# Optimization experiments

Hardware: AMD Instinct MI355X
Metric: run time of the kernel (lower is better)

## Reference

```python
import jax, jax.numpy as jnp
import numpy as np

EMBED_DIM = 528
NUM_HEADS = 8
HEAD_DIM = EMBED_DIM // NUM_HEADS  # 66


def setup_inputs() -> dict:
    key = jax.random.key(0)
    k1, k2, k3, k4, k5 = jax.random.split(key, 5)
    B, D, H, W, C = 1, 16, 16, 16, EMBED_DIM
    s = 1.0 / np.sqrt(C)
    return {
        "x": jax.random.normal(k1, (B, D, H, W, C), dtype=jnp.float32),
        "w_qkv": jax.random.uniform(k2, (3 * C, C), dtype=jnp.float32, minval=-s, maxval=s),
        "b_qkv": jax.random.uniform(k3, (3 * C,), dtype=jnp.float32, minval=-s, maxval=s),
        "w_proj": jax.random.uniform(k4, (C, C), dtype=jnp.float32, minval=-s, maxval=s),
        "b_proj": jax.random.uniform(k5, (C,), dtype=jnp.float32, minval=-s, maxval=s),
    }


def reference(x, w_qkv, b_qkv, w_proj, b_proj):
    B, D, H, W, C = x.shape
    N = D * H * W
    h, hd = NUM_HEADS, HEAD_DIM
    scaling = hd ** (-0.5)

    xt = x.reshape(B, N, C)
    # qkv projection: [B, N, 3C] -> [3, B, h, N, hd]
    qkv = xt @ w_qkv.T + b_qkv
    qkv = qkv.reshape(B, N, 3, h, hd).transpose(2, 0, 3, 1, 4)
    q, k, v = qkv[0], qkv[1], qkv[2]

    # full attention over all D*H*W tokens
    attn = jnp.einsum('bhqd,bhkd->bhqk', q, k) * scaling
    attn = jax.nn.softmax(attn, axis=-1)
    out = jnp.einsum('bhqk,bhkd->bhqd', attn, v)  # [B, h, N, hd]

    out = out.transpose(0, 2, 1, 3).reshape(B, N, h * hd)
    out = out @ w_proj.T + b_proj
    return out.reshape(B, D, H, W, C)
```

## Files before the change

### kernel.cpp

```cpp
#include <hip/hip_runtime.h>

typedef __attribute__((ext_vector_type(8))) short bf16x8;
typedef __attribute__((ext_vector_type(4))) float f32x4;
typedef __attribute__((ext_vector_type(16))) float f32x16;

#define DEV __device__ __forceinline__

static constexpr int N_TOK = 4096;
static constexpr int C     = 528;
static constexpr int NH    = 8;
static constexpr int HD    = 66;
static constexpr int HDP   = 96;
static constexpr int VD96  = 96;
static constexpr int KP    = 544;
static constexpr int NQKV  = 1584;
static constexpr int NQKVP = 1632;

DEV unsigned short f2bf(float f) {
    unsigned int u = __float_as_uint(f);
    u = (u + 0x7fffu + ((u >> 16) & 1u)) >> 16;
    return (unsigned short)u;
}
DEV float bf2f(unsigned short h) { return __uint_as_float(((unsigned int)h) << 16); }
DEV unsigned cvtpk2(float a, float b) {
    unsigned r;
    asm("v_cvt_pk_bf16_f32 %0, %1, %2" : "=v"(r) : "v"(a), "v"(b));
    return r;
}
DEV void plswap(unsigned &a, unsigned &b) {
    asm volatile("v_permlane32_swap_b32 %0, %1" : "+v"(a), "+v"(b));
}

__global__ void k_prep_all(const float* __restrict__ x, const float* __restrict__ w_qkv,
                           const float* __restrict__ w_proj,
                           unsigned short* __restrict__ xb, unsigned short* __restrict__ wqkvb,
                           unsigned short* __restrict__ whi, unsigned short* __restrict__ wlo,
                           unsigned short* __restrict__ qb, unsigned short* __restrict__ kbuf) {
    const int T0 = N_TOK * KP;
    const int T1 = T0 + NQKVP * KP;
    const int T2 = T1 + KP * KP;
    const int T3 = T2 + NH * N_TOK * (HDP - HD);
    for (int idx = blockIdx.x * 256 + threadIdx.x; idx < T3; idx += gridDim.x * 256) {
        if (idx < T0) {
            int n = idx / KP, k = idx - n * KP;
            xb[idx] = (k < C) ? f2bf(x[n * C + k]) : (unsigned short)0;
        } else if (idx < T1) {
            int j = idx - T0;
            int n = j / KP, k = j - n * KP;
            wqkvb[j] = (n < NQKV && k < C) ? f2bf(w_qkv[n * C + k]) : (unsigned short)0;
        } else if (idx < T2) {
            int j = idx - T1;
            int n = j / KP, k = j - n * KP;
            unsigned short hi = 0, lo = 0;
            if (n < C && k < C) {
                float v = w_proj[n * C + k];
                hi = f2bf(v);
                lo = f2bf(v - bf2f(hi));
            }
            whi[j] = hi; wlo[j] = lo;
        } else {
            int j = idx - T2;
            int n = j / 30, p = j - 30 * n;
            size_t a = (size_t)n * HDP + HD + p;
            qb[a] = 0; kbuf[a] = 0;
        }
    }
}

__launch_bounds__(256)
__global__ void k_gemm_qkv(const unsigned short* __restrict__ A,
                           const unsigned short* __restrict__ B,
                           const float* __restrict__ bias,
                           unsigned short* __restrict__ qb, unsigned short* __restrict__ kbuf,
                           unsigned short* __restrict__ vtmp) {
    constexpr int LDA = 40;
    __shared__ unsigned short Al[2][128 * LDA];
    __shared__ unsigned short Bl[2][96 * LDA];
    int tid = threadIdx.x, lane = tid & 63, wid = tid >> 6;
    int m0 = blockIdx.x * 128, n0 = blockIdx.y * 96;
    int wm = (wid >> 1) * 64, wn = (wid & 1) * 48;
    int arow0 = tid >> 2, arow1 = (256 + tid) >> 2, akc = (tid & 3) * 8;
    bool bhave = tid < 128;
    int brow1 = (256 + tid) >> 2;
    f32x4 acc[4][3] = {};
    bf16x8 ra0, ra1, rb0, rb1;

    ra0 = *(const bf16x8*)&A[(size_t)(m0 + arow0) * KP + akc];
    ra1 = *(const bf16x8*)&A[(size_t)(m0 + arow1) * KP + akc];
    rb0 = *(const bf16x8*)&B[(size_t)(n0 + arow0) * KP + akc];
    if (bhave) rb1 = *(const bf16x8*)&B[(size_t)(n0 + brow1) * KP + akc];
    *(bf16x8*)&Al[0][arow0 * LDA + akc] = ra0;
    *(bf16x8*)&Al[0][arow1 * LDA + akc] = ra1;
    *(bf16x8*)&Bl[0][arow0 * LDA + akc] = rb0;
    if (bhave) *(bf16x8*)&Bl[0][brow1 * LDA + akc] = rb1;
    __syncthreads();

    int kk = (lane >> 4) * 8, cc = lane & 15;
    for (int kt = 0; kt < 17; kt++) {
        int cur = kt & 1;
        if (kt < 16) {
            int k0 = (kt + 1) * 32;
            ra0 = *(const bf16x8*)&A[(size_t)(m0 + arow0) * KP + k0 + akc];
            ra1 = *(const bf16x8*)&A[(size_t)(m0 + arow1) * KP + k0 + akc];
            rb0 = *(const bf16x8*)&B[(size_t)(n0 + arow0) * KP + k0 + akc];
            if (bhave) rb1 = *(const bf16x8*)&B[(size_t)(n0 + brow1) * KP + k0 + akc];
        }
        bf16x8 af[4], bfr[3];
#pragma unroll
        for (int mi = 0; mi < 4; mi++) af[mi] = *(const bf16x8*)&Al[cur][(wm + mi * 16 + cc) * LDA + kk];
#pragma unroll
        for (int ni = 0; ni < 3; ni++) bfr[ni] = *(const bf16x8*)&Bl[cur][(wn + ni * 16 + cc) * LDA + kk];
#pragma unroll
        for (int mi = 0; mi < 4; mi++)
#pragma unroll
            for (int ni = 0; ni < 3; ni++)
                acc[mi][ni] = __builtin_amdgcn_mfma_f32_16x16x32_bf16(af[mi], bfr[ni], acc[mi][ni], 0, 0, 0);
        if (kt < 16) {
            int nxt = cur ^ 1;
            *(bf16x8*)&Al[nxt][arow0 * LDA + akc] = ra0;
            *(bf16x8*)&Al[nxt][arow1 * LDA + akc] = ra1;
            *(bf16x8*)&Bl[nxt][arow0 * LDA + akc] = rb0;
            if (bhave) *(bf16x8*)&Bl[nxt][brow1 * LDA + akc] = rb1;
        }
        __syncthreads();
    }
#pragma unroll
    for (int mi = 0; mi < 4; mi++)
#pragma unroll
        for (int ni = 0; ni < 3; ni++)
#pragma unroll
            for (int r = 0; r < 4; r++) {
                int row = m0 + wm + mi * 16 + (lane >> 4) * 4 + r;
                int col = n0 + wn + ni * 16 + cc;
                float v = acc[mi][ni][r] + (col < NQKV ? bias[col] : 0.f);
                unsigned short b = f2bf(v);
                if (col < 2 * C) {
                    int d5 = (col >= C) ? col - C : col;
                    unsigned h = (unsigned)d5 / 66u;
                    int dd = d5 - 66 * (int)h;
                    size_t a = ((size_t)h * N_TOK + row) * HDP + dd;
                    if (col >= C) kbuf[a] = b; else qb[a] = b;
                } else if (col < NQKV) {
                    vtmp[(size_t)row * C + (col - 2 * C)] = b;
                }
            }
}

__global__ void k_reshape_v(const unsigned short* __restrict__ vtmp, unsigned short* __restrict__ vt) {
    __shared__ unsigned short lt[64 * 104];
    int h = blockIdx.y, n0 = blockIdx.x * 64, tid = threadIdx.x;
#pragma unroll
    for (int i = 0; i < 24; i++) {
        int idx = i * 256 + tid;
        int ni = idx / 96, d = idx - ni * 96;
        unsigned short v = 0;
        if (d < HD) v = vtmp[(size_t)(n0 + ni) * C + h * HD + d];
        lt[ni * 104 + d] = v;
    }
    __syncthreads();
#pragma unroll
    for (int i = 0; i < 24; i++) {
        int idx = i * 256 + tid;
        int d = idx >> 6, ni = idx & 63;
        vt[((size_t)h * VD96 + d) * N_TOK + n0 + ni] = lt[ni * 104 + d];
    }
}

__launch_bounds__(1024, 4)
__global__ void k_attn(const unsigned short* __restrict__ qb,
                       const unsigned short* __restrict__ kb,
                       const unsigned short* __restrict__ vt,
                       unsigned short* __restrict__ ahi,
                       unsigned short* __restrict__ alo) {
    __shared__ __align__(16) unsigned short S[2][128 * 128 + 96 * 128];
    int tid = threadIdx.x, lane = tid & 63, wid = tid >> 6;
    int wq = wid & 3, kh = wid >> 2;
    int hi = lane >> 5, lq = lane & 31;
    int bid = blockIdx.x;
    int head = bid & 7;
    int q0 = (bid >> 3) * 128;
    const float SC2 = 0.12309149097933274f * 1.4426950408889634f;

    bf16x8 aq[6];
    {
        const unsigned short* qrow = qb + ((size_t)head * N_TOK + q0 + wq * 32 + lq) * HDP + hi * 8;
#pragma unroll
        for (int t = 0; t < 6; t++) aq[t] = *(const bf16x8*)&qrow[t * 16];
    }
    f32x16 o0 = {}, o1 = {}, o2 = {};
    float m_r = -3e38f, l_r = 0.f;

    const unsigned short* kg = kb + (size_t)head * N_TOK * HDP;
    const unsigned short* vg = vt + (size_t)head * VD96 * N_TOK;

    const unsigned short* gptr[3];
    int gstep[3], laddr[3];
#pragma unroll
    for (int j = 0; j < 3; j++) {
        int c = j * 1024 + tid;
        if (c < 1536) {
            int row = c / 12, ch = c - row * 12;
            gptr[j] = kg + (size_t)row * HDP + ch * 8;
            gstep[j] = 128 * HDP;
            laddr[j] = row * 128 + ((ch ^ (row & 15)) << 3);
        } else {
            int c2 = c - 1536;
            int row = c2 >> 4, ch = c2 & 15;
            gptr[j] = vg + (size_t)row * N_TOK + ch * 8;
            gstep[j] = 128;
            laddr[j] = 128 * 128 + row * 128 + ((ch ^ (row & 15)) << 3);
        }
    }
#pragma unroll
    for (int j = 0; j < 3; j++) {
        *(bf16x8*)&S[0][laddr[j]] = *(const bf16x8*)gptr[j];
        gptr[j] += gstep[j];
    }
    __syncthreads();

    for (int kt = 0; kt < 32; kt++) {
        int cur = kt & 1;
        bf16x8 g[3];
        if (kt < 31) {
#pragma unroll
            for (int j = 0; j < 3; j++) { g[j] = *(const bf16x8*)gptr[j]; gptr[j] += gstep[j]; }
        }

        f32x16 s0 = {};
        {
            int r0 = kh * 32 + lq;
            const unsigned short* Kc = &S[cur][0];
#pragma unroll
            for (int t = 0; t < 6; t++) {
                bf16x8 ka = *(const bf16x8*)&Kc[r0 * 128 + (((2 * t + hi) ^ (r0 & 15)) << 3)];
                s0 = __builtin_amdgcn_mfma_f32_32x32x16_bf16(ka, aq[t], s0, 0, 0, 0);
            }
        }

        float mx = s0[0];
#pragma unroll
        for (int r = 1; r < 16; r++) mx = fmaxf(mx, s0[r]);
        mx = fmaxf(mx, __shfl_xor(mx, 32, 64));
        if (!__all((mx - m_r) * SC2 <= 8.f)) {
            float mnew = fmaxf(m_r, mx);
            float fct = __builtin_amdgcn_exp2f((m_r - mnew) * SC2);
            m_r = mnew;
            l_r *= fct;
#pragma unroll
            for (int r = 0; r < 16; r++) { o0[r] *= fct; o1[r] *= fct; o2[r] *= fct; }
        }
        float nb = m_r * SC2;
        float lsum = 0.f;
#pragma unroll
        for (int r = 0; r < 16; r++) { s0[r] = __builtin_amdgcn_exp2f(__builtin_fmaf(s0[r], SC2, -nb)); lsum += s0[r]; }
        lsum += __shfl_xor(lsum, 32, 64);
        l_r += lsum;

        unsigned u0[4], u1[4];
#pragma unroll
        for (int a = 0; a < 4; a++) {
            u0[a] = cvtpk2(s0[4 * a + 0], s0[4 * a + 1]);
            u1[a] = cvtpk2(s0[4 * a + 2], s0[4 * a + 3]);
        }
        plswap(u0[0], u0[1]); plswap(u0[2], u0[3]);
        plswap(u1[0], u1[1]); plswap(u1[2], u1[3]);

        {
            const unsigned short* Vc = &S[cur][128 * 128];
#pragma unroll
            for (int t2 = 0; t2 < 2; t2++) {
                int a0 = t2 * 2;
                union { unsigned u[4]; bf16x8 v; } pf;
                pf.u[0] = u0[a0];     pf.u[1] = u1[a0];
                pf.u[2] = u0[a0 + 1]; pf.u[3] = u1[a0 + 1];
                int ch = kh * 4 + 2 * t2 + hi;
                int rv0 = lq, rv1 = 32 + lq, rv2 = 64 + lq;
                bf16x8 va0 = *(const bf16x8*)&Vc[rv0 * 128 + ((ch ^ (rv0 & 15)) << 3)];
                bf16x8 va1 = *(const bf16x8*)&Vc[rv1 * 128 + ((ch ^ (rv1 & 15)) << 3)];
                bf16x8 va2 = *(const bf16x8*)&Vc[rv2 * 128 + ((ch ^ (rv2 & 15)) << 3)];
                o0 = __builtin_amdgcn_mfma_f32_32x32x16_bf16(va0, pf.v, o0, 0, 0, 0);
                o1 = __builtin_amdgcn_mfma_f32_32x32x16_bf16(va1, pf.v, o1, 0, 0, 0);
                o2 = __builtin_amdgcn_mfma_f32_32x32x16_bf16(va2, pf.v, o2, 0, 0, 0);
            }
        }

        if (kt < 31) {
            int nxt = cur ^ 1;
#pragma unroll
            for (int j = 0; j < 3; j++) *(bf16x8*)&S[nxt][laddr[j]] = g[j];
        }
        __syncthreads();
    }

    float* xc = (float*)&S[0][0];
    {
        float* rg = xc + (size_t)((wq * 2 + (kh & 1)) * 64 + lane) * 53;
        if (kh >= 2) {
#pragma unroll
            for (int r = 0; r < 16; r++) { rg[r] = o0[r]; rg[16 + r] = o1[r]; rg[32 + r] = o2[r]; }
            rg[48] = m_r; rg[49] = l_r;
        }
        __syncthreads();
        if (kh < 2) {
            float m1 = rg[48], l1 = rg[49];
            float m12 = fmaxf(m_r, m1);
            float f0 = __builtin_amdgcn_exp2f((m_r - m12) * SC2);
            float f1 = __builtin_amdgcn_exp2f((m1 - m12) * SC2);
            l_r = l_r * f0 + l1 * f1;
            m_r = m12;
#pragma unroll
            for (int r = 0; r < 16; r++) {
                o0[r] = o0[r] * f0 + rg[r] * f1;
                o1[r] = o1[r] * f0 + rg[16 + r] * f1;
                o2[r] = o2[r] * f0 + rg[32 + r] * f1;
            }
        }
        __syncthreads();
    }
    {
        float* rg = xc + (size_t)(wq * 64 + lane) * 53;
        if (kh == 1) {
#pragma unroll
            for (int r = 0; r < 16; r++) { rg[r] = o0[r]; rg[16 + r] = o1[r]; rg[32 + r] = o2[r]; }
            rg[48] = m_r; rg[49] = l_r;
        }
        __syncthreads();
        if (kh == 0) {
            float m1 = rg[48], l1 = rg[49];
            float m12 = fmaxf(m_r, m1);
            float f0 = __builtin_amdgcn_exp2f((m_r - m12) * SC2);
            float f1 = __builtin_amdgcn_exp2f((m1 - m12) * SC2);
            float inv = 1.f / (l_r * f0 + l1 * f1);
            int token = q0 + wq * 32 + lq;
#pragma unroll
            for (int db = 0; db < 3; db++) {
#pragma unroll
                for (int r = 0; r < 16; r++) {
                    int d = db * 32 + (r & 3) + 8 * (r >> 2) + 4 * hi;
                    if (d < HD) {
                        float own = (db == 0) ? o0[r] : (db == 1) ? o1[r] : o2[r];
                        float val = (own * f0 + rg[db * 16 + r] * f1) * inv;
                        unsigned short hb = f2bf(val);
                        float lo = val - bf2f(hb);
                        size_t a = (size_t)token * KP + head * HD + d;
                        ahi[a] = hb; alo[a] = f2bf(lo);
                    }
                }
            }
        }
    }
}

__launch_bounds__(256)
__global__ void k_gemm_proj(const unsigned short* __restrict__ Ahi_, const unsigned short* __restrict__ Alo_,
                            const unsigned short* __restrict__ Whi_, const unsigned short* __restrict__ Wlo_,
                            const float* __restrict__ bias, float* __restrict__ out) {
    constexpr int LDA = 40;
    __shared__ unsigned short Ah[2][128 * LDA], Aw[2][128 * LDA];
    __shared__ unsigned short Bh[2][64 * LDA],  Bw[2][64 * LDA];
    int tid = threadIdx.x, lane = tid & 63, wid = tid >> 6;
    int m0 = blockIdx.x * 128, n0 = blockIdx.y * 64;
    int wm = wid * 32;
    int arow0 = tid >> 2, arow1 = (256 + tid) >> 2, akc = (tid & 3) * 8;
    bool bok = (n0 + arow0) < KP;
    f32x4 acc[2][4] = {};
    bf16x8 rah0, rah1, ral0, ral1, rbh, rbl;
    const bf16x8 zero8 = {};

    rah0 = *(const bf16x8*)&Ahi_[(size_t)(m0 + arow0) * KP + akc];
    rah1 = *(const bf16x8*)&Ahi_[(size_t)(m0 + arow1) * KP + akc];
    ral0 = *(const bf16x8*)&Alo_[(size_t)(m0 + arow0) * KP + akc];
    ral1 = *(const bf16x8*)&Alo_[(size_t)(m0 + arow1) * KP + akc];
    rbh = bok ? *(const bf16x8*)&Whi_[(size_t)(n0 + arow0) * KP + akc] : zero8;
    rbl = bok ? *(const bf16x8*)&Wlo_[(size_t)(n0 + arow0) * KP + akc] : zero8;
    *(bf16x8*)&Ah[0][arow0 * LDA + akc] = rah0;
    *(bf16x8*)&Ah[0][arow1 * LDA + akc] = rah1;
    *(bf16x8*)&Aw[0][arow0 * LDA + akc] = ral0;
    *(bf16x8*)&Aw[0][arow1 * LDA + akc] = ral1;
    *(bf16x8*)&Bh[0][arow0 * LDA + akc] = rbh;
    *(bf16x8*)&Bw[0][arow0 * LDA + akc] = rbl;
    __syncthreads();

    int kk = (lane >> 4) * 8, cc = lane & 15;
    for (int kt = 0; kt < 17; kt++) {
        int cur = kt & 1;
        if (kt < 16) {
            int k0 = (kt + 1) * 32;
            rah0 = *(const bf16x8*)&Ahi_[(size_t)(m0 + arow0) * KP + k0 + akc];
            rah1 = *(const bf16x8*)&Ahi_[(size_t)(m0 + arow1) * KP + k0 + akc];
            ral0 = *(const bf16x8*)&Alo_[(size_t)(m0 + arow0) * KP + k0 + akc];
            ral1 = *(const bf16x8*)&Alo_[(size_t)(m0 + arow1) * KP + k0 + akc];
            rbh = bok ? *(const bf16x8*)&Whi_[(size_t)(n0 + arow0) * KP + k0 + akc] : zero8;
            rbl = bok ? *(const bf16x8*)&Wlo_[(size_t)(n0 + arow0) * KP + k0 + akc] : zero8;
        }
        bf16x8 ah[2], al[2], bh[4], bl[4];
#pragma unroll
        for (int mi = 0; mi < 2; mi++) {
            ah[mi] = *(const bf16x8*)&Ah[cur][(wm + mi * 16 + cc) * LDA + kk];
            al[mi] = *(const bf16x8*)&Aw[cur][(wm + mi * 16 + cc) * LDA + kk];
        }
#pragma unroll
        for (int ni = 0; ni < 4; ni++) {
            bh[ni] = *(const bf16x8*)&Bh[cur][(ni * 16 + cc) * LDA + kk];
            bl[ni] = *(const bf16x8*)&Bw[cur][(ni * 16 + cc) * LDA + kk];
        }
#pragma unroll
        for (int mi = 0; mi < 2; mi++)
#pragma unroll
            for (int ni = 0; ni < 4; ni++) {
                acc[mi][ni] = __builtin_amdgcn_mfma_f32_16x16x32_bf16(ah[mi], bh[ni], acc[mi][ni], 0, 0, 0);
                acc[mi][ni] = __builtin_amdgcn_mfma_f32_16x16x32_bf16(ah[mi], bl[ni], acc[mi][ni], 0, 0, 0);
                acc[mi][ni] = __builtin_amdgcn_mfma_f32_16x16x32_bf16(al[mi], bh[ni], acc[mi][ni], 0, 0, 0);
            }
        if (kt < 16) {
            int nxt = cur ^ 1;
            *(bf16x8*)&Ah[nxt][arow0 * LDA + akc] = rah0;
            *(bf16x8*)&Ah[nxt][arow1 * LDA + akc] = rah1;
            *(bf16x8*)&Aw[nxt][arow0 * LDA + akc] = ral0;
            *(bf16x8*)&Aw[nxt][arow1 * LDA + akc] = ral1;
            *(bf16x8*)&Bh[nxt][arow0 * LDA + akc] = rbh;
            *(bf16x8*)&Bw[nxt][arow0 * LDA + akc] = rbl;
        }
        __syncthreads();
    }
#pragma unroll
    for (int mi = 0; mi < 2; mi++)
#pragma unroll
        for (int ni = 0; ni < 4; ni++)
#pragma unroll
            for (int r = 0; r < 4; r++) {
                int row = m0 + wm + mi * 16 + (lane >> 4) * 4 + r;
                int col = n0 + ni * 16 + cc;
                if (col < C) out[(size_t)row * C + col] = acc[mi][ni][r] + bias[col];
            }
}

extern "C" void kernel_launch(void* const* d_in, const int* in_sizes, int n_in,
                              void* d_out, int out_size, void* d_ws, size_t ws_size,
                              hipStream_t stream) {
    const float* x      = (const float*)d_in[0];
    const float* w_qkv  = (const float*)d_in[1];
    const float* b_qkv  = (const float*)d_in[2];
    const float* w_proj = (const float*)d_in[3];
    const float* b_proj = (const float*)d_in[4];
    float* out = (float*)d_out;
    char* ws = (char*)d_ws;

    const size_t o_xb    = 0;
    const size_t o_wqkvb = o_xb    + 4456448;
    const size_t o_whi   = o_wqkvb + 1775616;
    const size_t o_wlo   = o_whi   + 591872;
    const size_t o_vtmp  = o_wlo   + 591872;
    const size_t o_qbf   = o_vtmp  + 4456448;
    const size_t o_kbf   = o_qbf   + 6291456;
    const size_t o_vt    = o_kbf   + 6291456;
    const size_t need    = o_vt + 6291456;
    if (ws_size < need) return;

    unsigned short* xb    = (unsigned short*)(ws + o_xb);
    unsigned short* wqkvb = (unsigned short*)(ws + o_wqkvb);
    unsigned short* whi   = (unsigned short*)(ws + o_whi);
    unsigned short* wlo   = (unsigned short*)(ws + o_wlo);
    unsigned short* vtmp  = (unsigned short*)(ws + o_vtmp);
    unsigned short* qbf   = (unsigned short*)(ws + o_qbf);
    unsigned short* kbf   = (unsigned short*)(ws + o_kbf);
    unsigned short* vt    = (unsigned short*)(ws + o_vt);
    unsigned short* ahi   = xb;
    unsigned short* alo   = vtmp;

    k_prep_all  <<<2048, 256, 0, stream>>>(x, w_qkv, w_proj, xb, wqkvb, whi, wlo, qbf, kbf);
    k_gemm_qkv  <<<dim3(N_TOK / 128, NQKVP / 96), 256, 0, stream>>>(xb, wqkvb, b_qkv, qbf, kbf, vtmp);
    k_reshape_v <<<dim3(N_TOK / 64, NH), 256, 0, stream>>>(vtmp, vt);
    k_attn      <<<dim3(256), 1024, 0, stream>>>(qbf, kbf, vt, ahi, alo);
    k_gemm_proj <<<dim3(N_TOK / 128, 9), 256, 0, stream>>>(ahi, alo, whi, wlo, b_proj, out);
}
```

Before: 152.0 us.

## Split attention into 512 blocks of 64 queries with single-buffered LDS

Adds a new attention kernel in which each 512-thread block handles 64 query rows instead of 128, doubling the grid to 512 blocks across the 256 CUs. The K/V tile moves from a double buffer to a single LDS buffer with a barrier before and after the refill, halving shared memory per block so more blocks can be resident. Each K/V tile is now loaded from global memory twice as often in total, and the extra barrier exposes load latency. The old k_attn is left gutted and unused.

```diff
diff --git a/kernel.cpp b/kernel.cpp
--- a/kernel.cpp
+++ b/kernel.cpp
@@ -166,24 +166,33 @@
     }
 }
 
-__launch_bounds__(1024, 4)
+__launch_bounds__(512, 4)
 __global__ void k_attn(const unsigned short* __restrict__ qb,
                        const unsigned short* __restrict__ kb,
                        const unsigned short* __restrict__ vt,
                        unsigned short* __restrict__ ahi,
                        unsigned short* __restrict__ alo) {
-    __shared__ __align__(16) unsigned short S[2][128 * 128 + 96 * 128];
+    __shared__ __align__(16) unsigned short S[2][64 * 128 + 96 * 64];
     int tid = threadIdx.x, lane = tid & 63, wid = tid >> 6;
-    int wq = wid & 3, kh = wid >> 2;
+    int wq = wid & 1, kh = (wid >> 1) & 1;
+    int dup = wid >> 2;
+    wq = (wid & 1) | (dup << 1);
+    (void)dup;
+    wq = wid & 1;
+    int kq = wid >> 1;
+    kq = 0;
+    int qg = 0;
+    qg = wid & 1;
+    kh = wid >> 1;
     int hi = lane >> 5, lq = lane & 31;
     int bid = blockIdx.x;
     int head = bid & 7;
-    int q0 = (bid >> 3) * 128;
+    int q0 = (bid >> 3) * 64;
     const float SC2 = 0.12309149097933274f * 1.4426950408889634f;
 
     bf16x8 aq[6];
     {
-        const unsigned short* qrow = qb + ((size_t)head * N_TOK + q0 + wq * 32 + lq) * HDP + hi * 8;
+        const unsigned short* qrow = qb + ((size_t)head * N_TOK + q0 + qg * 32 + lq) * HDP + hi * 8;
 #pragma unroll
         for (int t = 0; t < 6; t++) aq[t] = *(const bf16x8*)&qrow[t * 16];
     }
@@ -193,46 +202,47 @@
     const unsigned short* kg = kb + (size_t)head * N_TOK * HDP;
     const unsigned short* vg = vt + (size_t)head * VD96 * N_TOK;
 
-    const unsigned short* gptr[3];
-    int gstep[3], laddr[3];
+    const unsigned short* gptrK[3];
+    const unsigned short* gptrV[3];
+    int laddrK[3], laddrV[3];
 #pragma unroll
     for (int j = 0; j < 3; j++) {
-        int c = j * 1024 + tid;
-        if (c < 1536) {
-            int row = c / 12, ch = c - row * 12;
-            gptr[j] = kg + (size_t)row * HDP + ch * 8;
-            gstep[j] = 128 * HDP;
-            laddr[j] = row * 128 + ((ch ^ (row & 15)) << 3);
-        } else {
-            int c2 = c - 1536;
-            int row = c2 >> 4, ch = c2 & 15;
-            gptr[j] = vg + (size_t)row * N_TOK + ch * 8;
-            gstep[j] = 128;
-            laddr[j] = 128 * 128 + row * 128 + ((ch ^ (row & 15)) << 3);
-        }
-    }
+        int c = j * 512 + tid;
+        int row = c / 12, ch = c - row * 12;
+        gptrK[j] = kg + (size_t)row * HDP + ch * 8;
+        laddrK[j] = row * 128 + ((ch ^ (row & 15)) << 3);
+        int row2 = c >> 4, ch2 = c & 15;
+        gptrV[j] = vg + (size_t)row2 * N_TOK + ch2 * 8;
+        laddrV[j] = 128 * 128 + row2 * 128 + ((ch2 ^ (row2 & 15)) << 3);
+    }
+    __shared__ __align__(16) unsigned short dummy[1];
+    (void)dummy;
+
 #pragma unroll
     for (int j = 0; j < 3; j++) {
-        *(bf16x8*)&S[0][laddr[j]] = *(const bf16x8*)gptr[j];
-        gptr[j] += gstep[j];
+        *(bf16x8*)&S[0][laddrK[j] - 0] = *(const bf16x8*)gptrK[j];
+        *(bf16x8*)&S[0][laddrV[j] - 128 * 128 + 64 * 128] = *(const bf16x8*)gptrV[j];
     }
     __syncthreads();
 
     for (int kt = 0; kt < 32; kt++) {
-        int cur = kt & 1;
-        bf16x8 g[3];
+        bf16x8 gk[3], gv[3];
         if (kt < 31) {
-#pragma unroll
-            for (int j = 0; j < 3; j++) { g[j] = *(const bf16x8*)gptr[j]; gptr[j] += gstep[j]; }
+            int n1 = (kt + 1) * 128;
+#pragma unroll
+            for (int j = 0; j < 3; j++) {
+                gk[j] = *(const bf16x8*)(gptrK[j] + (size_t)n1 * HDP);
+                gv[j] = *(const bf16x8*)(gptrV[j] + n1);
+            }
         }
 
         f32x16 s0 = {};
         {
             int r0 = kh * 32 + lq;
-            const unsigned short* Kc = &S[cur][0];
+            const unsigned short* Kc = &S[0][0];
 #pragma unroll
             for (int t = 0; t < 6; t++) {
-                bf16x8 ka = *(const bf16x8*)&Kc[r0 * 128 + (((2 * t + hi) ^ (r0 & 15)) << 3)];
+                bf16x8 ka = *(const bf16x8*)&Kc[(r0 & 63) * 128 + (((2 * t + hi) ^ (r0 & 15)) << 3) + (r0 >> 6) * (64 * 128 + 96 * 64)];
                 s0 = __builtin_amdgcn_mfma_f32_32x32x16_bf16(ka, aq[t], s0, 0, 0, 0);
             }
         }
@@ -266,7 +276,7 @@
         plswap(u1[0], u1[1]); plswap(u1[2], u1[3]);
 
         {
-            const unsigned short* Vc = &S[cur][128 * 128];
+            const unsigned short* Vc = &S[0][0];
 #pragma unroll
             for (int t2 = 0; t2 < 2; t2++) {
                 int a0 = t2 * 2;
@@ -275,80 +285,20 @@
                 pf.u[2] = u0[a0 + 1]; pf.u[3] = u1[a0 + 1];
                 int ch = kh * 4 + 2 * t2 + hi;
                 int rv0 = lq, rv1 = 32 + lq, rv2 = 64 + lq;
-                bf16x8 va0 = *(const bf16x8*)&Vc[rv0 * 128 + ((ch ^ (rv0 & 15)) << 3)];
-                bf16x8 va1 = *(const bf16x8*)&Vc[rv1 * 128 + ((ch ^ (rv1 & 15)) << 3)];
-                bf16x8 va2 = *(const bf16x8*)&Vc[rv2 * 128 + ((ch ^ (rv2 & 15)) << 3)];
-                o0 = __builtin_amdgcn_mfma_f32_32x32x16_bf16(va0, pf.v, o0, 0, 0, 0);
-                o1 = __builtin_amdgcn_mfma_f32_32x32x16_bf16(va1, pf.v, o1, 0, 0, 0);
-                o2 = __builtin_amdgcn_mfma_f32_32x32x16_bf16(va2, pf.v, o2, 0, 0, 0);
-            }
-        }
-
+                bf16x8 va0 = *(const bf16x8*)&Vc[64 * 128 + ((rv0 & 31) + (rv0 >> 5) * 0) * 0];
+                (void)va0; (void)rv1; (void)rv2; (void)ch; (void)pf;
+            }
+        }
         if (kt < 31) {
-            int nxt = cur ^ 1;
-#pragma unroll
-            for (int j = 0; j < 3; j++) *(bf16x8*)&S[nxt][laddr[j]] = g[j];
-        }
-        __syncthreads();
-    }
-
-    float* xc = (float*)&S[0][0];
-    {
-        float* rg = xc + (size_t)((wq * 2 + (kh & 1)) * 64 + lane) * 53;
-        if (kh >= 2) {
-#pragma unroll
-            for (int r = 0; r < 16; r++) { rg[r] = o0[r]; rg[16 + r] = o1[r]; rg[32 + r] = o2[r]; }
-            rg[48] = m_r; rg[49] = l_r;
-        }
-        __syncthreads();
-        if (kh < 2) {
-            float m1 = rg[48], l1 = rg[49];
-            float m12 = fmaxf(m_r, m1);
-            float f0 = __builtin_amdgcn_exp2f((m_r - m12) * SC2);
-            float f1 = __builtin_amdgcn_exp2f((m1 - m12) * SC2);
-            l_r = l_r * f0 + l1 * f1;
-            m_r = m12;
-#pragma unroll
-            for (int r = 0; r < 16; r++) {
-                o0[r] = o0[r] * f0 + rg[r] * f1;
-                o1[r] = o1[r] * f0 + rg[16 + r] * f1;
-                o2[r] = o2[r] * f0 + rg[32 + r] * f1;
-            }
-        }
-        __syncthreads();
-    }
-    {
-        float* rg = xc + (size_t)(wq * 64 + lane) * 53;
-        if (kh == 1) {
-#pragma unroll
-            for (int r = 0; r < 16; r++) { rg[r] = o0[r]; rg[16 + r] = o1[r]; rg[32 + r] = o2[r]; }
-            rg[48] = m_r; rg[49] = l_r;
-        }
-        __syncthreads();
-        if (kh == 0) {
-            float m1 = rg[48], l1 = rg[49];
-            float m12 = fmaxf(m_r, m1);
-            float f0 = __builtin_amdgcn_exp2f((m_r - m12) * SC2);
-            float f1 = __builtin_amdgcn_exp2f((m1 - m12) * SC2);
-            float inv = 1.f / (l_r * f0 + l1 * f1);
-            int token = q0 + wq * 32 + lq;
-#pragma unroll
-            for (int db = 0; db < 3; db++) {
-#pragma unroll
-                for (int r = 0; r < 16; r++) {
-                    int d = db * 32 + (r & 3) + 8 * (r >> 2) + 4 * hi;
-                    if (d < HD) {
-                        float own = (db == 0) ? o0[r] : (db == 1) ? o1[r] : o2[r];
-                        float val = (own * f0 + rg[db * 16 + r] * f1) * inv;
-                        unsigned short hb = f2bf(val);
-                        float lo = val - bf2f(hb);
-                        size_t a = (size_t)token * KP + head * HD + d;
-                        ahi[a] = hb; alo[a] = f2bf(lo);
-                    }
-                }
-            }
-        }
-    }
+#pragma unroll
+            for (int j = 0; j < 3; j++) {
+                *(bf16x8*)&S[0][laddrK[j]] = gk[j];
+                *(bf16x8*)&S[0][laddrV[j] - 128 * 128 + 64 * 128] = gv[j];
+            }
+        }
+        __syncthreads();
+    }
+    (void)o0; (void)o1; (void)o2; (void)m_r; (void)l_r; (void)ahi; (void)alo; (void)q0;
 }
 
 __launch_bounds__(256)
@@ -435,6 +385,189 @@
             }
 }
 
+__launch_bounds__(512, 4)
+__global__ void k_attn2(const unsigned short* __restrict__ qb,
+                        const unsigned short* __restrict__ kb,
+                        const unsigned short* __restrict__ vt,
+                        unsigned short* __restrict__ ahi,
+                        unsigned short* __restrict__ alo) {
+    __shared__ __align__(16) unsigned short S[128 * 128 + 96 * 128];
+    int tid = threadIdx.x, lane = tid & 63, wid = tid >> 6;
+    int qg = wid & 1;
+    int kh = wid >> 1;
+    int hi = lane >> 5, lq = lane & 31;
+    int bid = blockIdx.x;
+    int head = bid & 7;
+    int q0 = (bid >> 3) * 64;
+    const float SC2 = 0.12309149097933274f * 1.4426950408889634f;
+
+    bf16x8 aq[6];
+    {
+        const unsigned short* qrow = qb + ((size_t)head * N_TOK + q0 + qg * 32 + lq) * HDP + hi * 8;
+#pragma unroll
+        for (int t = 0; t < 6; t++) aq[t] = *(const bf16x8*)&qrow[t * 16];
+    }
+    f32x16 o0 = {}, o1 = {}, o2 = {};
+    float m_r = -3e38f, l_r = 0.f;
+
+    const unsigned short* kg = kb + (size_t)head * N_TOK * HDP;
+    const unsigned short* vg = vt + (size_t)head * VD96 * N_TOK;
+
+    const unsigned short* gpK[3];
+    const unsigned short* gpV[3];
+    int laK[3], laV[3];
+#pragma unroll
+    for (int j = 0; j < 3; j++) {
+        int c = j * 512 + tid;
+        int row = c / 12, ch = c - row * 12;
+        gpK[j] = kg + (size_t)row * HDP + ch * 8;
+        laK[j] = row * 128 + ((ch ^ (row & 15)) << 3);
+        int row2 = c >> 4, ch2 = c & 15;
+        gpV[j] = vg + (size_t)row2 * N_TOK + ch2 * 8;
+        laV[j] = 128 * 128 + row2 * 128 + ((ch2 ^ (row2 & 15)) << 3);
+    }
+#pragma unroll
+    for (int j = 0; j < 3; j++) {
+        *(bf16x8*)&S[laK[j]] = *(const bf16x8*)gpK[j];
+        *(bf16x8*)&S[laV[j]] = *(const bf16x8*)gpV[j];
+    }
+    __syncthreads();
+
+    for (int kt = 0; kt < 32; kt++) {
+        bf16x8 gk[3], gv[3];
+        if (kt < 31) {
+            size_t n1 = (size_t)(kt + 1) * 128;
+#pragma unroll
+            for (int j = 0; j < 3; j++) {
+                gk[j] = *(const bf16x8*)(gpK[j] + n1 * HDP);
+                gv[j] = *(const bf16x8*)(gpV[j] + n1);
+            }
+        }
+
+        f32x16 s0 = {};
+        {
+            int r0 = kh * 32 + lq;
+#pragma unroll
+            for (int t = 0; t < 6; t++) {
+                bf16x8 ka = *(const bf16x8*)&S[r0 * 128 + (((2 * t + hi) ^ (r0 & 15)) << 3)];
+                s0 = __builtin_amdgcn_mfma_f32_32x32x16_bf16(ka, aq[t], s0, 0, 0, 0);
+            }
+        }
+
+        float mx = s0[0];
+#pragma unroll
+        for (int r = 1; r < 16; r++) mx = fmaxf(mx, s0[r]);
+        mx = fmaxf(mx, __shfl_xor(mx, 32, 64));
+        if (!__all((mx - m_r) * SC2 <= 8.f)) {
+            float mnew = fmaxf(m_r, mx);
+            float fct = __builtin_amdgcn_exp2f((m_r - mnew) * SC2);
+            m_r = mnew;
+            l_r *= fct;
+#pragma unroll
+            for (int r = 0; r < 16; r++) { o0[r] *= fct; o1[r] *= fct; o2[r] *= fct; }
+        }
+        float nb = m_r * SC2;
+        float lsum = 0.f;
+#pragma unroll
+        for (int r = 0; r < 16; r++) { s0[r] = __builtin_amdgcn_exp2f(__builtin_fmaf(s0[r], SC2, -nb)); lsum += s0[r]; }
+        lsum += __shfl_xor(lsum, 32, 64);
+        l_r += lsum;
+
+        unsigned u0[4], u1[4];
+#pragma unroll
+        for (int a = 0; a < 4; a++) {
+            u0[a] = cvtpk2(s0[4 * a + 0], s0[4 * a + 1]);
+            u1[a] = cvtpk2(s0[4 * a + 2], s0[4 * a + 3]);
+        }
+        plswap(u0[0], u0[1]); plswap(u0[2], u0[3]);
+        plswap(u1[0], u1[1]); plswap(u1[2], u1[3]);
+
+#pragma unroll
+        for (int t2 = 0; t2 < 2; t2++) {
+            int a0 = t2 * 2;
+            union { unsigned u[4]; bf16x8 v; } pf;
+            pf.u[0] = u0[a0];     pf.u[1] = u1[a0];
+            pf.u[2] = u0[a0 + 1]; pf.u[3] = u1[a0 + 1];
+            int ch = kh * 4 + 2 * t2 + hi;
+            int rv0 = lq, rv1 = 32 + lq, rv2 = 64 + lq;
+            bf16x8 va0 = *(const bf16x8*)&S[128 * 128 + rv0 * 128 + ((ch ^ (rv0 & 15)) << 3)];
+            bf16x8 va1 = *(const bf16x8*)&S[128 * 128 + rv1 * 128 + ((ch ^ (rv1 & 15)) << 3)];
+            bf16x8 va2 = *(const bf16x8*)&S[128 * 128 + rv2 * 128 + ((ch ^ (rv2 & 15)) << 3)];
+            o0 = __builtin_amdgcn_mfma_f32_32x32x16_bf16(va0, pf.v, o0, 0, 0, 0);
+            o1 = __builtin_amdgcn_mfma_f32_32x32x16_bf16(va1, pf.v, o1, 0, 0, 0);
+            o2 = __builtin_amdgcn_mfma_f32_32x32x16_bf16(va2, pf.v, o2, 0, 0, 0);
+        }
+
+        __syncthreads();
+        if (kt < 31) {
+#pragma unroll
+            for (int j = 0; j < 3; j++) {
+                *(bf16x8*)&S[laK[j]] = gk[j];
+                *(bf16x8*)&S[laV[j]] = gv[j];
+            }
+        }
+        __syncthreads();
+    }
+
+    float* xc = (float*)&S[0];
+    {
+        float* rg = xc + (size_t)(((qg * 2 + (kh & 1)) * 64 + lane) * 53);
+        if (kh >= 2) {
+#pragma unroll
+            for (int r = 0; r < 16; r++) { rg[r] = o0[r]; rg[16 + r] = o1[r]; rg[32 + r] = o2[r]; }
+            rg[48] = m_r; rg[49] = l_r;
+        }
+        __syncthreads();
+        if (kh < 2) {
+            float m1 = rg[48], l1 = rg[49];
+            float m12 = fmaxf(m_r, m1);
+            float f0 = __builtin_amdgcn_exp2f((m_r - m12) * SC2);
+            float f1 = __builtin_amdgcn_exp2f((m1 - m12) * SC2);
+            l_r = l_r * f0 + l1 * f1;
+            m_r = m12;
+#pragma unroll
+            for (int r = 0; r < 16; r++) {
+                o0[r] = o0[r] * f0 + rg[r] * f1;
+                o1[r] = o1[r] * f0 + rg[16 + r] * f1;
+                o2[r] = o2[r] * f0 + rg[32 + r] * f1;
+            }
+        }
+        __syncthreads();
+    }
+    {
+        float* rg = xc + (size_t)((qg * 64 + lane) * 53);
+        if (kh == 1) {
+#pragma unroll
+            for (int r = 0; r < 16; r++) { rg[r] = o0[r]; rg[16 + r] = o1[r]; rg[32 + r] = o2[r]; }
+            rg[48] = m_r; rg[49] = l_r;
+        }
+        __syncthreads();
+        if (kh == 0) {
+            float m1 = rg[48], l1 = rg[49];
+            float m12 = fmaxf(m_r, m1);
+            float f0 = __builtin_amdgcn_exp2f((m_r - m12) * SC2);
+            float f1 = __builtin_amdgcn_exp2f((m1 - m12) * SC2);
+            float inv = 1.f / (l_r * f0 + l1 * f1);
+            int token = q0 + qg * 32 + lq;
+#pragma unroll
+            for (int db = 0; db < 3; db++) {
+#pragma unroll
+                for (int r = 0; r < 16; r++) {
+                    int d = db * 32 + (r & 3) + 8 * (r >> 2) + 4 * hi;
+                    if (d < HD) {
+                        float own = (db == 0) ? o0[r] : (db == 1) ? o1[r] : o2[r];
+                        float val = (own * f0 + rg[db * 16 + r] * f1) * inv;
+                        unsigned short hb = f2bf(val);
+                        float lo = val - bf2f(hb);
+                        size_t a = (size_t)token * KP + head * HD + d;
+                        ahi[a] = hb; alo[a] = f2bf(lo);
+                    }
+                }
+            }
+        }
+    }
+}
+
 extern "C" void kernel_launch(void* const* d_in, const int* in_sizes, int n_in,
                               void* d_out, int out_size, void* d_ws, size_t ws_size,
                               hipStream_t stream) {
@@ -471,6 +604,6 @@
     k_prep_all  <<<2048, 256, 0, stream>>>(x, w_qkv, w_proj, xb, wqkvb, whi, wlo, qbf, kbf);
     k_gemm_qkv  <<<dim3(N_TOK / 128, NQKVP / 96), 256, 0, stream>>>(xb, wqkvb, b_qkv, qbf, kbf, vtmp);
     k_reshape_v <<<dim3(N_TOK / 64, NH), 256, 0, stream>>>(vtmp, vt);
-    k_attn      <<<dim3(256), 1024, 0, stream>>>(qbf, kbf, vt, ahi, alo);
+    k_attn2     <<<dim3(512), 512, 0, stream>>>(qbf, kbf, vt, ahi, alo);
     k_gemm_proj <<<dim3(N_TOK / 128, 9), 256, 0, stream>>>(ahi, alo, whi, wlo, b_proj, out);
 }
```

Result: slower. 218.5 us (+43.7%).

## Halve attention block to 512 threads with single-buffered LDS and two key-halves

Applied to the files above, without the earlier changes.

The attention kernel now runs 8 waves instead of 16. Each wave covers 64 keys per tile instead of 32, computing two score MFMAs per step, and the KV split drops from four key-quarters to two. The LDS K/V tile goes from double to single buffering, with an extra barrier before the overwrite. The final cross-wave merge shrinks to one stage. The aim is fewer waves doing redundant softmax work, less LDS per block and a shorter reduction, at the cost of less latency hiding and an extra sync per iteration.

```diff
diff --git a/kernel.cpp b/kernel.cpp
--- a/kernel.cpp
+++ b/kernel.cpp
@@ -166,15 +166,16 @@
     }
 }
 
-__launch_bounds__(1024, 4)
+__launch_bounds__(512, 2)
 __global__ void k_attn(const unsigned short* __restrict__ qb,
                        const unsigned short* __restrict__ kb,
                        const unsigned short* __restrict__ vt,
                        unsigned short* __restrict__ ahi,
                        unsigned short* __restrict__ alo) {
-    __shared__ __align__(16) unsigned short S[2][128 * 128 + 96 * 128];
+    __shared__ __align__(16) unsigned short S[128 * 128 + 96 * 128];
     int tid = threadIdx.x, lane = tid & 63, wid = tid >> 6;
-    int wq = wid & 3, kh = wid >> 2;
+    int wq = wid & 3;
+    int kh = wid >> 2;
     int hi = lane >> 5, lq = lane & 31;
     int bid = blockIdx.x;
     int head = bid & 7;
@@ -193,53 +194,54 @@
     const unsigned short* kg = kb + (size_t)head * N_TOK * HDP;
     const unsigned short* vg = vt + (size_t)head * VD96 * N_TOK;
 
-    const unsigned short* gptr[3];
-    int gstep[3], laddr[3];
+    const unsigned short* gpK[3];
+    const unsigned short* gpV[3];
+    int laK[3], laV[3];
 #pragma unroll
     for (int j = 0; j < 3; j++) {
-        int c = j * 1024 + tid;
-        if (c < 1536) {
-            int row = c / 12, ch = c - row * 12;
-            gptr[j] = kg + (size_t)row * HDP + ch * 8;
-            gstep[j] = 128 * HDP;
-            laddr[j] = row * 128 + ((ch ^ (row & 15)) << 3);
-        } else {
-            int c2 = c - 1536;
-            int row = c2 >> 4, ch = c2 & 15;
-            gptr[j] = vg + (size_t)row * N_TOK + ch * 8;
-            gstep[j] = 128;
-            laddr[j] = 128 * 128 + row * 128 + ((ch ^ (row & 15)) << 3);
-        }
+        int c = j * 512 + tid;
+        int row = c / 12, ch = c - row * 12;
+        gpK[j] = kg + (size_t)row * HDP + ch * 8;
+        laK[j] = row * 128 + ((ch ^ (row & 15)) << 3);
+        int row2 = c >> 4, ch2 = c & 15;
+        gpV[j] = vg + (size_t)row2 * N_TOK + ch2 * 8;
+        laV[j] = 128 * 128 + row2 * 128 + ((ch2 ^ (row2 & 15)) << 3);
     }
 #pragma unroll
     for (int j = 0; j < 3; j++) {
-        *(bf16x8*)&S[0][laddr[j]] = *(const bf16x8*)gptr[j];
-        gptr[j] += gstep[j];
+        *(bf16x8*)&S[laK[j]] = *(const bf16x8*)gpK[j];
+        *(bf16x8*)&S[laV[j]] = *(const bf16x8*)gpV[j];
     }
     __syncthreads();
 
     for (int kt = 0; kt < 32; kt++) {
-        int cur = kt & 1;
-        bf16x8 g[3];
+        bf16x8 gk[3], gv[3];
         if (kt < 31) {
-#pragma unroll
-            for (int j = 0; j < 3; j++) { g[j] = *(const bf16x8*)gptr[j]; gptr[j] += gstep[j]; }
-        }
-
-        f32x16 s0 = {};
+            size_t n1 = (size_t)(kt + 1) * 128;
+#pragma unroll
+            for (int j = 0; j < 3; j++) {
+                gk[j] = *(const bf16x8*)(gpK[j] + n1 * HDP);
+                gv[j] = *(const bf16x8*)(gpV[j] + n1);
+            }
+        }
+
+        f32x16 s0 = {}, s1 = {};
         {
-            int r0 = kh * 32 + lq;
-            const unsigned short* Kc = &S[cur][0];
+            int r0 = kh * 64 + lq, r1 = r0 + 32;
 #pragma unroll
             for (int t = 0; t < 6; t++) {
-                bf16x8 ka = *(const bf16x8*)&Kc[r0 * 128 + (((2 * t + hi) ^ (r0 & 15)) << 3)];
-                s0 = __builtin_amdgcn_mfma_f32_32x32x16_bf16(ka, aq[t], s0, 0, 0, 0);
+                bf16x8 ka0 = *(const bf16x8*)&S[r0 * 128 + (((2 * t + hi) ^ (r0 & 15)) << 3)];
+                bf16x8 ka1 = *(const bf16x8*)&S[r1 * 128 + (((2 * t + hi) ^ (r1 & 15)) << 3)];
+                s0 = __builtin_amdgcn_mfma_f32_32x32x16_bf16(ka0, aq[t], s0, 0, 0, 0);
+                s1 = __builtin_amdgcn_mfma_f32_32x32x16_bf16(ka1, aq[t], s1, 0, 0, 0);
             }
         }
 
         float mx = s0[0];
 #pragma unroll
         for (int r = 1; r < 16; r++) mx = fmaxf(mx, s0[r]);
+#pragma unroll
+        for (int r = 0; r < 16; r++) mx = fmaxf(mx, s1[r]);
         mx = fmaxf(mx, __shfl_xor(mx, 32, 64));
         if (!__all((mx - m_r) * SC2 <= 8.f)) {
             float mnew = fmaxf(m_r, mx);
@@ -253,98 +255,81 @@
         float lsum = 0.f;
 #pragma unroll
         for (int r = 0; r < 16; r++) { s0[r] = __builtin_amdgcn_exp2f(__builtin_fmaf(s0[r], SC2, -nb)); lsum += s0[r]; }
+#pragma unroll
+        for (int r = 0; r < 16; r++) { s1[r] = __builtin_amdgcn_exp2f(__builtin_fmaf(s1[r], SC2, -nb)); lsum += s1[r]; }
         lsum += __shfl_xor(lsum, 32, 64);
         l_r += lsum;
 
-        unsigned u0[4], u1[4];
+        unsigned u0[2][4], u1[2][4];
 #pragma unroll
         for (int a = 0; a < 4; a++) {
-            u0[a] = cvtpk2(s0[4 * a + 0], s0[4 * a + 1]);
-            u1[a] = cvtpk2(s0[4 * a + 2], s0[4 * a + 3]);
-        }
-        plswap(u0[0], u0[1]); plswap(u0[2], u0[3]);
-        plswap(u1[0], u1[1]); plswap(u1[2], u1[3]);
-
-        {
-            const unsigned short* Vc = &S[cur][128 * 128];
-#pragma unroll
-            for (int t2 = 0; t2 < 2; t2++) {
-                int a0 = t2 * 2;
-                union { unsigned u[4]; bf16x8 v; } pf;
-                pf.u[0] = u0[a0];     pf.u[1] = u1[a0];
-                pf.u[2] = u0[a0 + 1]; pf.u[3] = u1[a0 + 1];
-                int ch = kh * 4 + 2 * t2 + hi;
-                int rv0 = lq, rv1 = 32 + lq, rv2 = 64 + lq;
-                bf16x8 va0 = *(const bf16x8*)&Vc[rv0 * 128 + ((ch ^ (rv0 & 15)) << 3)];
-                bf16x8 va1 = *(const bf16x8*)&Vc[rv1 * 128 + ((ch ^ (rv1 & 15)) << 3)];
-                bf16x8 va2 = *(const bf16x8*)&Vc[rv2 * 128 + ((ch ^ (rv2 & 15)) << 3)];
-                o0 = __builtin_amdgcn_mfma_f32_32x32x16_bf16(va0, pf.v, o0, 0, 0, 0);
-                o1 = __builtin_amdgcn_mfma_f32_32x32x16_bf16(va1, pf.v, o1, 0, 0, 0);
-                o2 = __builtin_amdgcn_mfma_f32_32x32x16_bf16(va2, pf.v, o2, 0, 0, 0);
-            }
-        }
-
+            u0[0][a] = cvtpk2(s0[4 * a + 0], s0[4 * a + 1]);
+            u1[0][a] = cvtpk2(s0[4 * a + 2], s0[4 * a + 3]);
+            u0[1][a] = cvtpk2(s1[4 * a + 0], s1[4 * a + 1]);
+            u1[1][a] = cvtpk2(s1[4 * a + 2], s1[4 * a + 3]);
+        }
+#pragma unroll
+        for (int kb2 = 0; kb2 < 2; kb2++)
+#pragma unroll
+            for (int a0 = 0; a0 < 4; a0 += 2) {
+                plswap(u0[kb2][a0], u0[kb2][a0 + 1]);
+                plswap(u1[kb2][a0], u1[kb2][a0 + 1]);
+            }
+
+#pragma unroll
+        for (int t2 = 0; t2 < 4; t2++) {
+            int kb2 = t2 >> 1, a0 = (t2 & 1) * 2;
+            union { unsigned u[4]; bf16x8 v; } pf;
+            pf.u[0] = u0[kb2][a0];     pf.u[1] = u1[kb2][a0];
+            pf.u[2] = u0[kb2][a0 + 1]; pf.u[3] = u1[kb2][a0 + 1];
+            int ch = kh * 8 + 2 * t2 + hi;
+            int rv0 = lq, rv1 = 32 + lq, rv2 = 64 + lq;
+            bf16x8 va0 = *(const bf16x8*)&S[128 * 128 + rv0 * 128 + ((ch ^ (rv0 & 15)) << 3)];
+            bf16x8 va1 = *(const bf16x8*)&S[128 * 128 + rv1 * 128 + ((ch ^ (rv1 & 15)) << 3)];
+            bf16x8 va2 = *(const bf16x8*)&S[128 * 128 + rv2 * 128 + ((ch ^ (rv2 & 15)) << 3)];
+            o0 = __builtin_amdgcn_mfma_f32_32x32x16_bf16(va0, pf.v, o0, 0, 0, 0);
+            o1 = __builtin_amdgcn_mfma_f32_32x32x16_bf16(va1, pf.v, o1, 0, 0, 0);
+            o2 = __builtin_amdgcn_mfma_f32_32x32x16_bf16(va2, pf.v, o2, 0, 0, 0);
+        }
+
+        __syncthreads();
         if (kt < 31) {
-            int nxt = cur ^ 1;
-#pragma unroll
-            for (int j = 0; j < 3; j++) *(bf16x8*)&S[nxt][laddr[j]] = g[j];
+#pragma unroll
+            for (int j = 0; j < 3; j++) {
+                *(bf16x8*)&S[laK[j]] = gk[j];
+                *(bf16x8*)&S[laV[j]] = gv[j];
+            }
         }
         __syncthreads();
     }
 
-    float* xc = (float*)&S[0][0];
-    {
-        float* rg = xc + (size_t)((wq * 2 + (kh & 1)) * 64 + lane) * 53;
-        if (kh >= 2) {
-#pragma unroll
-            for (int r = 0; r < 16; r++) { rg[r] = o0[r]; rg[16 + r] = o1[r]; rg[32 + r] = o2[r]; }
-            rg[48] = m_r; rg[49] = l_r;
-        }
-        __syncthreads();
-        if (kh < 2) {
-            float m1 = rg[48], l1 = rg[49];
-            float m12 = fmaxf(m_r, m1);
-            float f0 = __builtin_amdgcn_exp2f((m_r - m12) * SC2);
-            float f1 = __builtin_amdgcn_exp2f((m1 - m12) * SC2);
-            l_r = l_r * f0 + l1 * f1;
-            m_r = m12;
+    float* xc = (float*)&S[0];
+    float* rg = xc + (size_t)((wq * 64 + lane) * 52);
+    if (kh == 1) {
+#pragma unroll
+        for (int r = 0; r < 16; r++) { rg[r] = o0[r]; rg[16 + r] = o1[r]; rg[32 + r] = o2[r]; }
+        rg[48] = m_r; rg[49] = l_r;
+    }
+    __syncthreads();
+    if (kh == 0) {
+        float m1 = rg[48], l1 = rg[49];
+        float m12 = fmaxf(m_r, m1);
+        float f0 = __builtin_amdgcn_exp2f((m_r - m12) * SC2);
+        float f1 = __builtin_amdgcn_exp2f((m1 - m12) * SC2);
+        float inv = 1.f / (l_r * f0 + l1 * f1);
+        int token = q0 + wq * 32 + lq;
+#pragma unroll
+        for (int db = 0; db < 3; db++) {
 #pragma unroll
             for (int r = 0; r < 16; r++) {
-                o0[r] = o0[r] * f0 + rg[r] * f1;
-                o1[r] = o1[r] * f0 + rg[16 + r] * f1;
-                o2[r] = o2[r] * f0 + rg[32 + r] * f1;
-            }
-        }
-        __syncthreads();
-    }
-    {
-        float* rg = xc + (size_t)(wq * 64 + lane) * 53;
-        if (kh == 1) {
-#pragma unroll
-            for (int r = 0; r < 16; r++) { rg[r] = o0[r]; rg[16 + r] = o1[r]; rg[32 + r] = o2[r]; }
-            rg[48] = m_r; rg[49] = l_r;
-        }
-        __syncthreads();
-        if (kh == 0) {
-            float m1 = rg[48], l1 = rg[49];
-            float m12 = fmaxf(m_r, m1);
-            float f0 = __builtin_amdgcn_exp2f((m_r - m12) * SC2);
-            float f1 = __builtin_amdgcn_exp2f((m1 - m12) * SC2);
-            float inv = 1.f / (l_r * f0 + l1 * f1);
-            int token = q0 + wq * 32 + lq;
-#pragma unroll
-            for (int db = 0; db < 3; db++) {
-#pragma unroll
-                for (int r = 0; r < 16; r++) {
-                    int d = db * 32 + (r & 3) + 8 * (r >> 2) + 4 * hi;
-                    if (d < HD) {
-                        float own = (db == 0) ? o0[r] : (db == 1) ? o1[r] : o2[r];
-                        float val = (own * f0 + rg[db * 16 + r] * f1) * inv;
-                        unsigned short hb = f2bf(val);
-                        float lo = val - bf2f(hb);
-                        size_t a = (size_t)token * KP + head * HD + d;
-                        ahi[a] = hb; alo[a] = f2bf(lo);
-                    }
+                int d = db * 32 + (r & 3) + 8 * (r >> 2) + 4 * hi;
+                if (d < HD) {
+                    float own = (db == 0) ? o0[r] : (db == 1) ? o1[r] : o2[r];
+                    float val = (own * f0 + rg[db * 16 + r] * f1) * inv;
+                    unsigned short hb = f2bf(val);
+                    float lo = val - bf2f(hb);
+                    size_t a = (size_t)token * KP + head * HD + d;
+                    ahi[a] = hb; alo[a] = f2bf(lo);
                 }
             }
         }
@@ -471,6 +456,6 @@
     k_prep_all  <<<2048, 256, 0, stream>>>(x, w_qkv, w_proj, xb, wqkvb, whi, wlo, qbf, kbf);
     k_gemm_qkv  <<<dim3(N_TOK / 128, NQKVP / 96), 256, 0, stream>>>(xb, wqkvb, b_qkv, qbf, kbf, vtmp);
     k_reshape_v <<<dim3(N_TOK / 64, NH), 256, 0, stream>>>(vtmp, vt);
-    k_attn      <<<dim3(256), 1024, 0, stream>>>(qbf, kbf, vt, ahi, alo);
+    k_attn      <<<dim3(256), 512, 0, stream>>>(qbf, kbf, vt, ahi, alo);
     k_gemm_proj <<<dim3(N_TOK / 128, 9), 256, 0, stream>>>(ahi, alo, whi, wlo, b_proj, out);
 }
```

Measured after the change: 129.4 us. 1.17x faster.
